# Performance work log

Measured on AMD Instinct MI355X. Metric: run time of the kernel, lower is better.

The kernel has to match this reference:

```python
import jax, jax.numpy as jnp
import numpy as np

NUM_HEADS = 16
EPS = 1e-06


def setup_inputs() -> dict:
    key = jax.random.key(0)
    ks = jax.random.split(key, 6)
    b, s, d = 4, 4096, 1024
    scale = 1.0 / np.sqrt(d)
    return {
        "x": jax.random.normal(ks[0], (b, s, d), dtype=jnp.float32),
        "wq": jax.random.normal(ks[1], (d, d), dtype=jnp.float32) * scale,
        "wk": jax.random.normal(ks[2], (d, d), dtype=jnp.float32) * scale,
        "wv": jax.random.normal(ks[3], (d, d), dtype=jnp.float32) * scale,
        "wo": jax.random.normal(ks[4], (d, d), dtype=jnp.float32) * scale,
        "bo": jnp.zeros((d,), dtype=jnp.float32),
    }


def _split_heads(t, h):
    b, s, d = t.shape
    return t.reshape(b, s, h, d // h).transpose(0, 2, 1, 3)  # [b,h,s,dh]


def reference(x, wq, wk, wv, wo, bo):
    h = NUM_HEADS
    # torch Linear: y = x @ W.T (no bias for q/k/v)
    q = _split_heads(x @ wq.T, h)
    k = _split_heads(x @ wk.T, h)
    v = _split_heads(x @ wv.T, h)
    # ELU+1 feature map
    qf = jax.nn.elu(q) + 1.0
    kf = jax.nn.elu(k) + 1.0
    # global key feature sum over sequence: [b,h,dh]
    k_sum = jnp.sum(kf, axis=-2)
    # denominator: [b,h,s,1]
    denom = jnp.sum(qf * k_sum[:, :, None, :], axis=-1, keepdims=True) + EPS
    # kv = sum_s kf_s (outer) v_s  -> [b,h,dh,dh]  (the broadcast-sum in torch == matmul)
    kv = jnp.einsum('bhsd,bhse->bhde', kf, v)
    # q_kv: [b,h,s,dh]
    q_kv = jnp.einsum('bhsd,bhde->bhse', qf, kv)
    out = q_kv / denom
    b, _, s, dh = out.shape
    out = out.transpose(0, 2, 1, 3).reshape(b, s, h * dh)  # merge heads
    return out @ wo.T + bo
```

## Files before the change

### kernel.cpp

```cpp
#include <hip/hip_runtime.h>
#include <hip/hip_bf16.h>
#include <cmath>


#define TOK    16384
#define DMODEL 1024
#define NHEAD  16
#define DH     64
#define KSPLIT 8

using bf16x8 = __attribute__((ext_vector_type(8))) short;
using f32x4  = __attribute__((ext_vector_type(4))) float;

typedef __attribute__((address_space(1))) const unsigned int gld_src_t;
typedef __attribute__((address_space(3))) unsigned int gld_dst_t;

__device__ __forceinline__ unsigned short f2bf(float x) {
    unsigned int u = __float_as_uint(x);
    u += 0x7fffu + ((u >> 16) & 1u);
    return (unsigned short)(u >> 16);
}
__device__ __forceinline__ float bf2f(unsigned short b) {
    return __uint_as_float((unsigned int)b << 16);
}

__global__ __launch_bounds__(256) void split_k(
    const float* __restrict__ in, unsigned short* __restrict__ hi,
    unsigned short* __restrict__ lo, int n)
{
    int i = (blockIdx.x * 256 + threadIdx.x) * 4;
    if (i >= n) return;
    float4 v = *(const float4*)(in + i);
    float vs[4] = {v.x, v.y, v.z, v.w};
    unsigned short hh[4], ll[4];
#pragma unroll
    for (int j = 0; j < 4; ++j) {
        unsigned short h = f2bf(vs[j]);
        hh[j] = h;
        ll[j] = f2bf(vs[j] - bf2f(h));
    }
    *(ushort4*)(hi + i) = make_ushort4(hh[0], hh[1], hh[2], hh[3]);
    *(ushort4*)(lo + i) = make_ushort4(ll[0], ll[1], ll[2], ll[3]);
}

__global__ __launch_bounds__(256) void splitw_k(
    const float* __restrict__ w0, const float* __restrict__ w1,
    const float* __restrict__ w2, const float* __restrict__ w3,
    unsigned short* __restrict__ hs, unsigned short* __restrict__ ls)
{
    int w = blockIdx.x >> 10;
    const float* src = (w == 0) ? w0 : (w == 1) ? w1 : (w == 2) ? w2 : w3;
    int i = ((blockIdx.x & 1023) * 256 + threadIdx.x) * 4;
    size_t base = (size_t)w * (DMODEL * DMODEL);
    float4 v = *(const float4*)(src + i);
    float vs[4] = {v.x, v.y, v.z, v.w};
    unsigned short hh[4], ll[4];
#pragma unroll
    for (int j = 0; j < 4; ++j) {
        unsigned short h = f2bf(vs[j]);
        hh[j] = h;
        ll[j] = f2bf(vs[j] - bf2f(h));
    }
    *(ushort4*)(hs + base + i) = make_ushort4(hh[0], hh[1], hh[2], hh[3]);
    *(ushort4*)(ls + base + i) = make_ushort4(ll[0], ll[1], ll[2], ll[3]);
}

template<int ACT>
__global__ __launch_bounds__(512, 2) void gemm256_k(
    const unsigned short* __restrict__ Ah, const unsigned short* __restrict__ Al,
    const unsigned short* __restrict__ Bh, const unsigned short* __restrict__ Bl,
    const float* __restrict__ bias, float* __restrict__ C,
    unsigned short* __restrict__ Ch, unsigned short* __restrict__ Cl,
    int M, int N, int K)
{
    __shared__ unsigned short lds[2][4][256 * 32];
    const int tid  = threadIdx.x;
    const int lane = tid & 63, wid = tid >> 6;

    const int nwg = gridDim.x, cpx = nwg >> 3;
    const int g = ((int)blockIdx.x & 7) * cpx + ((int)blockIdx.x >> 3);
    const int m0 = (g >> 2) * 256, n0 = (g & 3) * 256;

    const int wr = wid >> 2, wc = wid & 3;
    const int fr = lane & 15, ko = lane >> 4;

    f32x4 acc[8][4];
#pragma unroll
    for (int i = 0; i < 8; ++i)
#pragma unroll
        for (int j = 0; j < 4; ++j) acc[i][j] = (f32x4){0.f, 0.f, 0.f, 0.f};

    const unsigned short* srcb = (wid < 2) ? Ah : (wid < 4) ? Al : (wid < 6) ? Bh : Bl;
    const int rowbase = ((wid < 4) ? m0 : n0) + (wid & 1) * 128;
    const int rloc = (wid & 1) * 128 + (lane >> 2);
    const int sslot = (lane & 3) ^ ((rloc >> 1) & 3);
    const unsigned short* gsrc0 = srcb + (size_t)(rowbase + (lane >> 2)) * K + sslot * 8;
    const int mat  = wid >> 1;
    const int ldso = ((wid & 1) * 128) * 32;

    const int koff = (ko ^ ((fr >> 1) & 3)) * 8;
    const int nt = K / 32;

#pragma unroll
    for (int t = 0; t < 8; ++t) {
        __builtin_amdgcn_global_load_lds((gld_src_t*)(gsrc0 + (size_t)t * 16 * K),
            (gld_dst_t*)&lds[0][mat][ldso + t * 512], 16, 0, 0);
    }
    __syncthreads();

    for (int t = 0; t < nt; ++t) {
        const int cur = t & 1;
        if (t + 1 < nt) {
            const unsigned short* gk = gsrc0 + (size_t)(t + 1) * 32;
#pragma unroll
            for (int u = 0; u < 8; ++u) {
                __builtin_amdgcn_global_load_lds((gld_src_t*)(gk + (size_t)u * 16 * K),
                    (gld_dst_t*)&lds[cur ^ 1][mat][ldso + u * 512], 16, 0, 0);
            }
        }
        bf16x8 ah[8], al[8];
#pragma unroll
        for (int mi = 0; mi < 8; ++mi) {
            int off = (wr * 128 + mi * 16 + fr) * 32 + koff;
            ah[mi] = *(const bf16x8*)&lds[cur][0][off];
            al[mi] = *(const bf16x8*)&lds[cur][1][off];
        }
#pragma unroll
        for (int nj = 0; nj < 4; ++nj) {
            int off = (wc * 64 + nj * 16 + fr) * 32 + koff;
            bf16x8 bh = *(const bf16x8*)&lds[cur][2][off];
            bf16x8 bl = *(const bf16x8*)&lds[cur][3][off];
#pragma unroll
            for (int mi = 0; mi < 8; ++mi) {
                acc[mi][nj] = __builtin_amdgcn_mfma_f32_16x16x32_bf16(ah[mi], bh, acc[mi][nj], 0, 0, 0);
                acc[mi][nj] = __builtin_amdgcn_mfma_f32_16x16x32_bf16(ah[mi], bl, acc[mi][nj], 0, 0, 0);
                acc[mi][nj] = __builtin_amdgcn_mfma_f32_16x16x32_bf16(al[mi], bh, acc[mi][nj], 0, 0, 0);
            }
        }
        __syncthreads();
    }

    const int fq = ko;
#pragma unroll
    for (int mi = 0; mi < 8; ++mi) {
#pragma unroll
        for (int i = 0; i < 4; ++i) {
            int m = m0 + wr * 128 + mi * 16 + fq * 4 + i;
            size_t rbase = (size_t)m * N + n0 + wc * 64;
#pragma unroll
            for (int nj = 0; nj < 4; ++nj) {
                int n = nj * 16 + fr;
                float v = acc[mi][nj][i];
                if (ACT == 1 || ACT == 3) v = (v > 0.f) ? (v + 1.f) : expf(v);
                if (ACT == 2) v += bias[n0 + wc * 64 + n];
                if (ACT == 3) {
                    unsigned short hb = f2bf(v);
                    Ch[rbase + n] = hb;
                    Cl[rbase + n] = f2bf(v - bf2f(hb));
                } else {
                    C[rbase + n] = v;
                }
            }
        }
    }
}

__global__ __launch_bounds__(256) void kv_partial_k(
    const float* __restrict__ kf, const float* __restrict__ vchunk,
    int bh_base, float* __restrict__ kvp, float* __restrict__ ksp)
{
    __shared__ float kfs[8][64];
    __shared__ float vs[8][64];
    const int bh = bh_base + blockIdx.x;
    const int split = blockIdx.y;
    const int b = bh >> 4, h = bh & 15;
    const int blocal = b - (bh_base >> 4);
    const int tid = threadIdx.x;
    const int col = tid & 63, rg = tid >> 6;
    const int tx = tid & 15, ty = tid >> 4;
    const int di0 = ty * 4, dj0 = tx * 4;

    float acc[4][4] = {};
    float ks[4] = {0.f, 0.f, 0.f, 0.f};

    const int rows = 4096 / KSPLIT;
    const size_t kbase = ((size_t)b * 4096 + (size_t)split * rows) * DMODEL + h * DH;
    const size_t vbase = ((size_t)blocal * 4096 + (size_t)split * rows) * DMODEL + h * DH;

    for (int it = 0; it < rows / 8; ++it) {
        __syncthreads();
#pragma unroll
        for (int p = 0; p < 2; ++p) {
            int r = rg + p * 4;
            size_t o = (size_t)(it * 8 + r) * DMODEL + col;
            kfs[r][col] = kf[kbase + o];
            vs[r][col]  = vchunk[vbase + o];
        }
        __syncthreads();
#pragma unroll
        for (int r = 0; r < 8; ++r) {
            float a[4], bb[4];
#pragma unroll
            for (int i = 0; i < 4; ++i) a[i] = kfs[r][di0 + i];
#pragma unroll
            for (int j = 0; j < 4; ++j) bb[j] = vs[r][dj0 + j];
#pragma unroll
            for (int i = 0; i < 4; ++i)
#pragma unroll
                for (int j = 0; j < 4; ++j)
                    acc[i][j] = fmaf(a[i], bb[j], acc[i][j]);
            if (tx == 0) {
#pragma unroll
                for (int i = 0; i < 4; ++i) ks[i] += a[i];
            }
        }
    }

    const size_t obase = ((size_t)(bh * KSPLIT + split)) * (DH * DH);
#pragma unroll
    for (int i = 0; i < 4; ++i)
#pragma unroll
        for (int j = 0; j < 4; ++j)
            kvp[obase + (size_t)(di0 + i) * DH + dj0 + j] = acc[i][j];
    if (tx == 0) {
        size_t kb = ((size_t)(bh * KSPLIT + split)) * DH + di0;
#pragma unroll
        for (int i = 0; i < 4; ++i) ksp[kb + i] = ks[i];
    }
}

__global__ __launch_bounds__(256) void reduce_kv_k(
    const float* __restrict__ kvp, const float* __restrict__ ksp,
    unsigned short* __restrict__ kvth, unsigned short* __restrict__ kvtl)
{
    int idx = blockIdx.x * 256 + threadIdx.x;
    int bh = idx >> 12, off = idx & 4095;
    int d = off & 63, e = off >> 6;
    float s = 0.f;
    for (int c = 0; c < KSPLIT; ++c) s += kvp[((size_t)(bh * KSPLIT + c)) * 4096 + d * 64 + e];
    unsigned short hb = f2bf(s);
    size_t o = (size_t)bh * (96 * 64) + (size_t)e * 64 + d;
    kvth[o] = hb;
    kvtl[o] = f2bf(s - bf2f(hb));
    if (idx < 64 * DH) {
        int bh2 = idx >> 6, d2 = idx & 63;
        float t = 0.f;
        for (int c = 0; c < KSPLIT; ++c) t += ksp[((size_t)(bh2 * KSPLIT + c)) * DH + d2];
        unsigned short h2 = f2bf(t);
        size_t o2 = (size_t)bh2 * (96 * 64) + 64 * 64 + d2;
        kvth[o2] = h2;
        kvtl[o2] = f2bf(t - bf2f(h2));
    }
}

__global__ __launch_bounds__(512, 2) void attn_mfma_k(
    const unsigned short* __restrict__ qh, const unsigned short* __restrict__ ql,
    const unsigned short* __restrict__ kvth, const unsigned short* __restrict__ kvtl,
    unsigned short* __restrict__ out_hi, unsigned short* __restrict__ out_lo)
{
    __shared__ unsigned short lds[28672];
    __shared__ float denoms[128];
    const int tid = threadIdx.x, lane = tid & 63, wid = tid >> 6;
    const int blk = blockIdx.x;
    const int bh = blk >> 5, tb = blk & 31;
    const int b = bh >> 4, h = bh & 15;
    const int t0 = b * 4096 + tb * 128;

    const int l8 = lane >> 3, s7 = lane & 7;
#pragma unroll
    for (int shot = 0; shot < 7; ++shot) {
        int r = wid * 7 + shot;
        const unsigned short* src;
        int dstE;
        if (r < 32) {
            int row = (r & 15) * 8 + l8;
            int sslot = s7 ^ (row & 7);
            src = ((r < 16) ? qh : ql) + (size_t)(t0 + row) * DMODEL + h * DH + sslot * 8;
            dstE = ((r < 16) ? 0 : 8192) + (r & 15) * 512;
        } else {
            int rb = r - 32;
            int rl = (rb < 12) ? rb : rb - 12;
            int row = rl * 8 + l8;
            int sslot = s7 ^ (row & 7);
            src = ((rb < 12) ? kvth : kvtl) + (size_t)bh * (96 * 64) + row * 64 + sslot * 8;
            dstE = ((rb < 12) ? 16384 : 22528) + rl * 512;
        }
        __builtin_amdgcn_global_load_lds((gld_src_t*)src, (gld_dst_t*)&lds[dstE], 16, 0, 0);
    }
    __syncthreads();

    const int fr = lane & 15, ko = lane >> 4, fq = ko;
    const int arow = wid * 16 + fr;

    f32x4 acc[5];
#pragma unroll
    for (int nj = 0; nj < 5; ++nj) acc[nj] = (f32x4){0.f, 0.f, 0.f, 0.f};

#pragma unroll
    for (int kt = 0; kt < 2; ++kt) {
        int aoff = arow * 64 + ((kt * 4 + ko) ^ (arow & 7)) * 8;
        bf16x8 a_h = *(const bf16x8*)&lds[aoff];
        bf16x8 a_l = *(const bf16x8*)&lds[8192 + aoff];
#pragma unroll
        for (int nj = 0; nj < 5; ++nj) {
            int brow = nj * 16 + fr;
            int boff = brow * 64 + ((kt * 4 + ko) ^ (brow & 7)) * 8;
            bf16x8 b_h = *(const bf16x8*)&lds[16384 + boff];
            bf16x8 b_l = *(const bf16x8*)&lds[22528 + boff];
            acc[nj] = __builtin_amdgcn_mfma_f32_16x16x32_bf16(a_h, b_h, acc[nj], 0, 0, 0);
            acc[nj] = __builtin_amdgcn_mfma_f32_16x16x32_bf16(a_h, b_l, acc[nj], 0, 0, 0);
            acc[nj] = __builtin_amdgcn_mfma_f32_16x16x32_bf16(a_l, b_h, acc[nj], 0, 0, 0);
        }
    }

    if (fr == 0) {
#pragma unroll
        for (int i = 0; i < 4; ++i)
            denoms[wid * 16 + fq * 4 + i] = acc[4][i] + 1e-6f;
    }
    __syncthreads();

#pragma unroll
    for (int i = 0; i < 4; ++i) {
        int row = wid * 16 + fq * 4 + i;
        float dinv = 1.0f / denoms[row];
        size_t rbase = (size_t)(t0 + row) * DMODEL + h * DH;
#pragma unroll
        for (int nj = 0; nj < 4; ++nj) {
            float v = acc[nj][i] * dinv;
            unsigned short hb = f2bf(v);
            out_hi[rbase + nj * 16 + fr] = hb;
            out_lo[rbase + nj * 16 + fr] = f2bf(v - bf2f(hb));
        }
    }
}

extern "C" void kernel_launch(void* const* d_in, const int* in_sizes, int n_in,
                              void* d_out, int out_size, void* d_ws, size_t ws_size,
                              hipStream_t stream)
{
    const float* x  = (const float*)d_in[0];
    const float* wq = (const float*)d_in[1];
    const float* wk = (const float*)d_in[2];
    const float* wv = (const float*)d_in[3];
    const float* wo = (const float*)d_in[4];
    const float* bo = (const float*)d_in[5];
    float* out = (float*)d_out;

    const size_t XE = (size_t)TOK * DMODEL;
    const size_t WE = (size_t)DMODEL * DMODEL;
    const size_t CE = (size_t)8192 * DMODEL;

    unsigned short* xh = (unsigned short*)d_ws;
    unsigned short* xl = xh + XE;
    unsigned short* wh = xl + XE;
    unsigned short* wl = wh + 4 * WE;
    float* kf   = (float*)(wl + 4 * WE);
    float* vc   = kf + XE;
    float* kvp  = vc + CE;
    float* ksp  = kvp + (size_t)64 * KSPLIT * DH * DH;
    unsigned short* kvth = (unsigned short*)(ksp + (size_t)64 * KSPLIT * DH);
    unsigned short* kvtl = kvth + (size_t)64 * 96 * 64;
    unsigned short* qh = (unsigned short*)kf;
    unsigned short* ql = qh + XE;

    split_k<<<(int)(XE / 1024), 256, 0, stream>>>(x, xh, xl, (int)XE);
    splitw_k<<<4096, 256, 0, stream>>>(wq, wk, wv, wo, wh, wl);

    const int gfull = (TOK / 256) * 4;
    const int ghalf = (8192 / 256) * 4;

    gemm256_k<1><<<gfull, 512, 0, stream>>>(xh, xl, wh + WE, wl + WE, nullptr, kf, nullptr, nullptr, TOK, DMODEL, DMODEL);

    gemm256_k<0><<<ghalf, 512, 0, stream>>>(xh, xl, wh + 2 * WE, wl + 2 * WE, nullptr, vc, nullptr, nullptr, 8192, DMODEL, DMODEL);
    kv_partial_k<<<dim3(32, KSPLIT), 256, 0, stream>>>(kf, vc, 0, kvp, ksp);

    gemm256_k<0><<<ghalf, 512, 0, stream>>>(xh + CE, xl + CE, wh + 2 * WE, wl + 2 * WE, nullptr, vc, nullptr, nullptr, 8192, DMODEL, DMODEL);
    kv_partial_k<<<dim3(32, KSPLIT), 256, 0, stream>>>(kf, vc, 32, kvp, ksp);

    reduce_kv_k<<<dim3(64 * DH * DH / 256), 256, 0, stream>>>(kvp, ksp, kvth, kvtl);

    gemm256_k<3><<<gfull, 512, 0, stream>>>(xh, xl, wh, wl, nullptr, nullptr, qh, ql, TOK, DMODEL, DMODEL);
    attn_mfma_k<<<2048, 512, 0, stream>>>(qh, ql, kvth, kvtl, xh, xl);

    gemm256_k<2><<<gfull, 512, 0, stream>>>(xh, xl, wh + 3 * WE, wl + 3 * WE, bo, out, nullptr, nullptr, TOK, DMODEL, DMODEL);
}
```

Measured before the change: 523.7 us.

## Interleave next-tile global-to-LDS loads with MFMA phases in GEMM main loop

The split-bf16 GEMM K-loop is restructured into four phases per tile. Each phase issues a slice of the next tile's global_load_lds, reads two A fragments from LDS and runs a block of MFMAs. B fragments are loaded once per tile. Explicit s_waitcnt vmcnt/lgkmcnt, raw s_barrier, sched_barrier and s_setprio replace __syncthreads, so memory traffic overlaps MFMA issue and waves are favoured while in the MFMA section. This adds several barriers per K-step, which can serialise waves, and relies on hand-counted vmcnt values being correct.

After: 553.6 us. 1.06x slower.

```diff
diff --git a/kernel.cpp b/kernel.cpp
--- a/kernel.cpp
+++ b/kernel.cpp
@@ -99,45 +99,69 @@
     const int ldso = ((wid & 1) * 128) * 32;
 
     const int koff = (ko ^ ((fr >> 1) & 3)) * 8;
+    const int abase = (wr * 128 + fr) * 32 + koff;
+    const int bbase = (wc * 64 + fr) * 32 + koff;
     const int nt = K / 32;
 
 #pragma unroll
-    for (int t = 0; t < 8; ++t) {
-        __builtin_amdgcn_global_load_lds((gld_src_t*)(gsrc0 + (size_t)t * 16 * K),
-            (gld_dst_t*)&lds[0][mat][ldso + t * 512], 16, 0, 0);
-    }
-    __syncthreads();
+    for (int u = 0; u < 8; ++u) {
+        __builtin_amdgcn_global_load_lds((gld_src_t*)(gsrc0 + (size_t)u * 16 * K),
+            (gld_dst_t*)&lds[0][mat][ldso + u * 512], 16, 0, 0);
+    }
+    asm volatile("s_waitcnt vmcnt(0)" ::: "memory");
+    __builtin_amdgcn_s_barrier();
 
     for (int t = 0; t < nt; ++t) {
         const int cur = t & 1;
-        if (t + 1 < nt) {
-            const unsigned short* gk = gsrc0 + (size_t)(t + 1) * 32;
-#pragma unroll
-            for (int u = 0; u < 8; ++u) {
-                __builtin_amdgcn_global_load_lds((gld_src_t*)(gk + (size_t)u * 16 * K),
-                    (gld_dst_t*)&lds[cur ^ 1][mat][ldso + u * 512], 16, 0, 0);
-            }
-        }
-        bf16x8 ah[8], al[8];
-#pragma unroll
-        for (int mi = 0; mi < 8; ++mi) {
-            int off = (wr * 128 + mi * 16 + fr) * 32 + koff;
-            ah[mi] = *(const bf16x8*)&lds[cur][0][off];
-            al[mi] = *(const bf16x8*)&lds[cur][1][off];
-        }
-#pragma unroll
-        for (int nj = 0; nj < 4; ++nj) {
-            int off = (wc * 64 + nj * 16 + fr) * 32 + koff;
-            bf16x8 bh = *(const bf16x8*)&lds[cur][2][off];
-            bf16x8 bl = *(const bf16x8*)&lds[cur][3][off];
-#pragma unroll
-            for (int mi = 0; mi < 8; ++mi) {
-                acc[mi][nj] = __builtin_amdgcn_mfma_f32_16x16x32_bf16(ah[mi], bh, acc[mi][nj], 0, 0, 0);
-                acc[mi][nj] = __builtin_amdgcn_mfma_f32_16x16x32_bf16(ah[mi], bl, acc[mi][nj], 0, 0, 0);
-                acc[mi][nj] = __builtin_amdgcn_mfma_f32_16x16x32_bf16(al[mi], bh, acc[mi][nj], 0, 0, 0);
-            }
-        }
-        __syncthreads();
+        const bool hv = (t + 1 < nt);
+        const unsigned short* gk = gsrc0 + (size_t)(t + 1) * 32;
+        unsigned short* ldsn = &lds[cur ^ 1][mat][ldso];
+        bf16x8 Bh_[4], Bl_[4];
+
+#pragma unroll
+        for (int p = 0; p < 4; ++p) {
+            if (hv) {
+#pragma unroll
+                for (int q = 0; q < 2; ++q) {
+                    int u = p * 2 + q;
+                    __builtin_amdgcn_global_load_lds((gld_src_t*)(gk + (size_t)u * 16 * K),
+                        (gld_dst_t*)(ldsn + u * 512), 16, 0, 0);
+                }
+            }
+            if (p == 0) {
+                if (hv) asm volatile("s_waitcnt vmcnt(2)" ::: "memory");
+                else    asm volatile("s_waitcnt vmcnt(0)" ::: "memory");
+                __builtin_amdgcn_s_barrier();
+            }
+            int aoff0 = abase + (2 * p) * 16 * 32;
+            bf16x8 ah0 = *(const bf16x8*)&lds[cur][0][aoff0];
+            bf16x8 al0 = *(const bf16x8*)&lds[cur][1][aoff0];
+            bf16x8 ah1 = *(const bf16x8*)&lds[cur][0][aoff0 + 512];
+            bf16x8 al1 = *(const bf16x8*)&lds[cur][1][aoff0 + 512];
+            if (p == 0) {
+#pragma unroll
+                for (int nj = 0; nj < 4; ++nj) {
+                    int boff = bbase + nj * 16 * 32;
+                    Bh_[nj] = *(const bf16x8*)&lds[cur][2][boff];
+                    Bl_[nj] = *(const bf16x8*)&lds[cur][3][boff];
+                }
+            }
+            __builtin_amdgcn_s_barrier();
+            asm volatile("s_waitcnt lgkmcnt(0)" ::: "memory");
+            __builtin_amdgcn_sched_barrier(0);
+            __builtin_amdgcn_s_setprio(1);
+#pragma unroll
+            for (int nj = 0; nj < 4; ++nj) {
+                acc[2*p  ][nj] = __builtin_amdgcn_mfma_f32_16x16x32_bf16(ah0, Bh_[nj], acc[2*p  ][nj], 0, 0, 0);
+                acc[2*p  ][nj] = __builtin_amdgcn_mfma_f32_16x16x32_bf16(ah0, Bl_[nj], acc[2*p  ][nj], 0, 0, 0);
+                acc[2*p  ][nj] = __builtin_amdgcn_mfma_f32_16x16x32_bf16(al0, Bh_[nj], acc[2*p  ][nj], 0, 0, 0);
+                acc[2*p+1][nj] = __builtin_amdgcn_mfma_f32_16x16x32_bf16(ah1, Bh_[nj], acc[2*p+1][nj], 0, 0, 0);
+                acc[2*p+1][nj] = __builtin_amdgcn_mfma_f32_16x16x32_bf16(ah1, Bl_[nj], acc[2*p+1][nj], 0, 0, 0);
+                acc[2*p+1][nj] = __builtin_amdgcn_mfma_f32_16x16x32_bf16(al1, Bh_[nj], acc[2*p+1][nj], 0, 0, 0);
+            }
+            __builtin_amdgcn_s_setprio(0);
+            __builtin_amdgcn_s_barrier();
+        }
     }
 
     const int fq = ko;
```

## Shrink GEMM tiles to 128x128 and load B fragments directly into registers

Applied to the files above, without the earlier changes.

Replaces the 256x256, 512-thread split-bf16 GEMM with a 128x128, 256-thread version. Only the A hi/lo tiles are staged through LDS. Each wave loads its B hi/lo fragments straight from global memory into registers and prefetches the next K step into registers. This cuts LDS footprint and LDS read traffic per block and allows more blocks in flight. The cost is lower arithmetic intensity per tile, more redundant global reads of the weight matrix, and uncoalesced 16-byte-per-lane B loads.

New measurement: 758.1 us. 44.8% more time.

```diff
diff --git a/kernel.cpp b/kernel.cpp
--- a/kernel.cpp
+++ b/kernel.cpp
@@ -66,86 +66,103 @@
 }
 
 template<int ACT>
-__global__ __launch_bounds__(512, 2) void gemm256_k(
+__global__ __launch_bounds__(256, 2) void gemmv3_k(
     const unsigned short* __restrict__ Ah, const unsigned short* __restrict__ Al,
     const unsigned short* __restrict__ Bh, const unsigned short* __restrict__ Bl,
     const float* __restrict__ bias, float* __restrict__ C,
     unsigned short* __restrict__ Ch, unsigned short* __restrict__ Cl,
     int M, int N, int K)
 {
-    __shared__ unsigned short lds[2][4][256 * 32];
-    const int tid  = threadIdx.x;
-    const int lane = tid & 63, wid = tid >> 6;
+    __shared__ unsigned short lds[2][2][128 * 32];
+    const int tid = threadIdx.x, lane = tid & 63, wid = tid >> 6;
 
     const int nwg = gridDim.x, cpx = nwg >> 3;
     const int g = ((int)blockIdx.x & 7) * cpx + ((int)blockIdx.x >> 3);
-    const int m0 = (g >> 2) * 256, n0 = (g & 3) * 256;
-
-    const int wr = wid >> 2, wc = wid & 3;
+    const int m0 = (g >> 3) * 128, n0 = (g & 7) * 128;
+
+    const int wr = wid >> 1, wc = wid & 1;
     const int fr = lane & 15, ko = lane >> 4;
 
-    f32x4 acc[8][4];
-#pragma unroll
-    for (int i = 0; i < 8; ++i)
+    f32x4 acc[4][4];
+#pragma unroll
+    for (int i = 0; i < 4; ++i)
 #pragma unroll
         for (int j = 0; j < 4; ++j) acc[i][j] = (f32x4){0.f, 0.f, 0.f, 0.f};
 
-    const unsigned short* srcb = (wid < 2) ? Ah : (wid < 4) ? Al : (wid < 6) ? Bh : Bl;
-    const int rowbase = ((wid < 4) ? m0 : n0) + (wid & 1) * 128;
-    const int rloc = (wid & 1) * 128 + (lane >> 2);
+    const int smat  = wid >> 1;
+    const int srow0 = (wid & 1) * 64;
+    const int rloc  = srow0 + (lane >> 2);
     const int sslot = (lane & 3) ^ ((rloc >> 1) & 3);
-    const unsigned short* gsrc0 = srcb + (size_t)(rowbase + (lane >> 2)) * K + sslot * 8;
-    const int mat  = wid >> 1;
-    const int ldso = ((wid & 1) * 128) * 32;
+    const unsigned short* gsA = ((smat == 0) ? Ah : Al)
+                              + (size_t)(m0 + rloc) * K + sslot * 8;
 
     const int koff = (ko ^ ((fr >> 1) & 3)) * 8;
+    const int brow = n0 + wc * 64 + fr;
+    const unsigned short* gBh = Bh + (size_t)brow * K + ko * 8;
+    const unsigned short* gBl = Bl + (size_t)brow * K + ko * 8;
+
     const int nt = K / 32;
 
 #pragma unroll
-    for (int t = 0; t < 8; ++t) {
-        __builtin_amdgcn_global_load_lds((gld_src_t*)(gsrc0 + (size_t)t * 16 * K),
-            (gld_dst_t*)&lds[0][mat][ldso + t * 512], 16, 0, 0);
+    for (int s = 0; s < 4; ++s) {
+        __builtin_amdgcn_global_load_lds((gld_src_t*)(gsA + (size_t)s * 16 * K),
+            (gld_dst_t*)&lds[0][smat][(srow0 + s * 16) * 32], 16, 0, 0);
+    }
+    bf16x8 bh[4], bl[4];
+#pragma unroll
+    for (int nj = 0; nj < 4; ++nj) {
+        bh[nj] = *(const bf16x8*)(gBh + (size_t)nj * 16 * K);
+        bl[nj] = *(const bf16x8*)(gBl + (size_t)nj * 16 * K);
     }
     __syncthreads();
 
     for (int t = 0; t < nt; ++t) {
         const int cur = t & 1;
-        if (t + 1 < nt) {
-            const unsigned short* gk = gsrc0 + (size_t)(t + 1) * 32;
-#pragma unroll
-            for (int u = 0; u < 8; ++u) {
-                __builtin_amdgcn_global_load_lds((gld_src_t*)(gk + (size_t)u * 16 * K),
-                    (gld_dst_t*)&lds[cur ^ 1][mat][ldso + u * 512], 16, 0, 0);
+        const bool hv = (t + 1 < nt);
+        if (hv) {
+#pragma unroll
+            for (int s = 0; s < 4; ++s) {
+                __builtin_amdgcn_global_load_lds(
+                    (gld_src_t*)(gsA + (size_t)(t + 1) * 32 + (size_t)s * 16 * K),
+                    (gld_dst_t*)&lds[cur ^ 1][smat][(srow0 + s * 16) * 32], 16, 0, 0);
             }
         }
-        bf16x8 ah[8], al[8];
-#pragma unroll
-        for (int mi = 0; mi < 8; ++mi) {
-            int off = (wr * 128 + mi * 16 + fr) * 32 + koff;
+        bf16x8 bhn[4], bln[4];
+        if (hv) {
+#pragma unroll
+            for (int nj = 0; nj < 4; ++nj) {
+                bhn[nj] = *(const bf16x8*)(gBh + (size_t)(t + 1) * 32 + (size_t)nj * 16 * K);
+                bln[nj] = *(const bf16x8*)(gBl + (size_t)(t + 1) * 32 + (size_t)nj * 16 * K);
+            }
+        }
+        bf16x8 ah[4], al[4];
+#pragma unroll
+        for (int mi = 0; mi < 4; ++mi) {
+            int off = (wr * 64 + mi * 16 + fr) * 32 + koff;
             ah[mi] = *(const bf16x8*)&lds[cur][0][off];
             al[mi] = *(const bf16x8*)&lds[cur][1][off];
         }
 #pragma unroll
-        for (int nj = 0; nj < 4; ++nj) {
-            int off = (wc * 64 + nj * 16 + fr) * 32 + koff;
-            bf16x8 bh = *(const bf16x8*)&lds[cur][2][off];
-            bf16x8 bl = *(const bf16x8*)&lds[cur][3][off];
-#pragma unroll
-            for (int mi = 0; mi < 8; ++mi) {
-                acc[mi][nj] = __builtin_amdgcn_mfma_f32_16x16x32_bf16(ah[mi], bh, acc[mi][nj], 0, 0, 0);
-                acc[mi][nj] = __builtin_amdgcn_mfma_f32_16x16x32_bf16(ah[mi], bl, acc[mi][nj], 0, 0, 0);
-                acc[mi][nj] = __builtin_amdgcn_mfma_f32_16x16x32_bf16(al[mi], bh, acc[mi][nj], 0, 0, 0);
+        for (int nj = 0; nj < 4; ++nj)
+#pragma unroll
+            for (int mi = 0; mi < 4; ++mi) {
+                acc[mi][nj] = __builtin_amdgcn_mfma_f32_16x16x32_bf16(ah[mi], bh[nj], acc[mi][nj], 0, 0, 0);
+                acc[mi][nj] = __builtin_amdgcn_mfma_f32_16x16x32_bf16(ah[mi], bl[nj], acc[mi][nj], 0, 0, 0);
+                acc[mi][nj] = __builtin_amdgcn_mfma_f32_16x16x32_bf16(al[mi], bh[nj], acc[mi][nj], 0, 0, 0);
             }
-        }
         __syncthreads();
+        if (hv) {
+#pragma unroll
+            for (int nj = 0; nj < 4; ++nj) { bh[nj] = bhn[nj]; bl[nj] = bln[nj]; }
+        }
     }
 
     const int fq = ko;
 #pragma unroll
-    for (int mi = 0; mi < 8; ++mi) {
+    for (int mi = 0; mi < 4; ++mi) {
 #pragma unroll
         for (int i = 0; i < 4; ++i) {
-            int m = m0 + wr * 128 + mi * 16 + fq * 4 + i;
+            int m = m0 + wr * 64 + mi * 16 + fq * 4 + i;
             size_t rbase = (size_t)m * N + n0 + wc * 64;
 #pragma unroll
             for (int nj = 0; nj < 4; ++nj) {
@@ -367,21 +384,21 @@
     split_k<<<(int)(XE / 1024), 256, 0, stream>>>(x, xh, xl, (int)XE);
     splitw_k<<<4096, 256, 0, stream>>>(wq, wk, wv, wo, wh, wl);
 
-    const int gfull = (TOK / 256) * 4;
-    const int ghalf = (8192 / 256) * 4;
-
-    gemm256_k<1><<<gfull, 512, 0, stream>>>(xh, xl, wh + WE, wl + WE, nullptr, kf, nullptr, nullptr, TOK, DMODEL, DMODEL);
-
-    gemm256_k<0><<<ghalf, 512, 0, stream>>>(xh, xl, wh + 2 * WE, wl + 2 * WE, nullptr, vc, nullptr, nullptr, 8192, DMODEL, DMODEL);
+    const int gfull = (TOK / 128) * 8;
+    const int ghalf = (8192 / 128) * 8;
+
+    gemmv3_k<1><<<gfull, 256, 0, stream>>>(xh, xl, wh + WE, wl + WE, nullptr, kf, nullptr, nullptr, TOK, DMODEL, DMODEL);
+
+    gemmv3_k<0><<<ghalf, 256, 0, stream>>>(xh, xl, wh + 2 * WE, wl + 2 * WE, nullptr, vc, nullptr, nullptr, 8192, DMODEL, DMODEL);
     kv_partial_k<<<dim3(32, KSPLIT), 256, 0, stream>>>(kf, vc, 0, kvp, ksp);
 
-    gemm256_k<0><<<ghalf, 512, 0, stream>>>(xh + CE, xl + CE, wh + 2 * WE, wl + 2 * WE, nullptr, vc, nullptr, nullptr, 8192, DMODEL, DMODEL);
+    gemmv3_k<0><<<ghalf, 256, 0, stream>>>(xh + CE, xl + CE, wh + 2 * WE, wl + 2 * WE, nullptr, vc, nullptr, nullptr, 8192, DMODEL, DMODEL);
     kv_partial_k<<<dim3(32, KSPLIT), 256, 0, stream>>>(kf, vc, 32, kvp, ksp);
 
     reduce_kv_k<<<dim3(64 * DH * DH / 256), 256, 0, stream>>>(kvp, ksp, kvth, kvtl);
 
-    gemm256_k<3><<<gfull, 512, 0, stream>>>(xh, xl, wh, wl, nullptr, nullptr, qh, ql, TOK, DMODEL, DMODEL);
+    gemmv3_k<3><<<gfull, 256, 0, stream>>>(xh, xl, wh, wl, nullptr, nullptr, qh, ql, TOK, DMODEL, DMODEL);
     attn_mfma_k<<<2048, 512, 0, stream>>>(qh, ql, kvth, kvtl, xh, xl);
 
-    gemm256_k<2><<<gfull, 512, 0, stream>>>(xh, xl, wh + 3 * WE, wl + 3 * WE, bo, out, nullptr, nullptr, TOK, DMODEL, DMODEL);
-}
+    gemmv3_k<2><<<gfull, 256, 0, stream>>>(xh, xl, wh + 3 * WE, wl + 3 * WE, bo, out, nullptr, nullptr, TOK, DMODEL, DMODEL);
+}
```
